# Kernel optimization log

Hardware: AMD Instinct MI355X
Metric: run time of the kernel (lower is better)

## Reference

```python
import jax, jax.numpy as jnp
import numpy as np

DEPTH, DIM, DFF, DT, VOCAB = 3, 512, 2048, 64, 32000
B, L = 2, 512


def setup_inputs() -> dict:
    key = jax.random.key(0)
    ks = jax.random.split(key, 16)
    z = lambda *s: jnp.zeros(s, jnp.float32)
    o = lambda *s: jnp.ones(s, jnp.float32)
    n = lambda k, s, std: jax.random.normal(k, s, jnp.float32) * std
    return {
        "x": jax.random.normal(ks[0], (B, L, VOCAB), jnp.float32),
        "tok_in_w": n(ks[1], (DIM, VOCAB), VOCAB ** -0.5),
        "tok_in_b": z(DIM),
        "ln1_g": o(DEPTH, DIM), "ln1_b": z(DEPTH, DIM),
        "fc_w": n(ks[2], (DEPTH, DT, DIM), DIM ** -0.5), "fc_b": z(DEPTH, DT),
        "tin_w": n(ks[3], (DEPTH, DT, DIM), DIM ** -0.5), "tin_b": z(DEPTH, DT),
        "a_w": n(ks[4], (DEPTH, 2 * DT, DT), DT ** -0.5),
        "h0": jax.random.normal(ks[5], (DEPTH, DT, 2), jnp.float32),
        "tout_w": n(ks[6], (DEPTH, DIM, DT), DT ** -0.5), "tout_b": z(DEPTH, DIM),
        "ln2_g": o(DEPTH, DIM), "ln2_b": z(DEPTH, DIM),
        "ffn_w1": n(ks[7], (DEPTH, DFF, DIM), DIM ** -0.5), "ffn_b1": z(DEPTH, DFF),
        "ffn_w2": n(ks[8], (DEPTH, DIM, DFF), DFF ** -0.5), "ffn_b2": z(DEPTH, DIM),
        "lnf_g": o(DIM), "lnf_b": z(DIM),
        "tok_out_w": n(ks[9], (VOCAB, DIM), DIM ** -0.5), "tok_out_b": z(VOCAB),
    }


def _ln(x, g, b, eps=1e-5):
    m = x.mean(-1, keepdims=True)
    v = jnp.mean((x - m) ** 2, -1, keepdims=True)
    return (x - m) * jax.lax.rsqrt(v + eps) * g + b


def _sioconv(x, a_w, h0):
    # x: (B, L, D). Complex decaying linear recurrence, materialized as the
    # same O(L^2) kernel the torch code builds (cumsum of complex logs replaces
    # the FFT-conv-with-ones, which computes exactly a prefix sum along k).
    Bx, Lx, D = x.shape
    za = (x @ a_w.T).reshape(Bx, Lx, D, 2)
    m2 = za[..., 0] ** 2 + za[..., 1] ** 2
    scale = jax.lax.rsqrt(m2) * jnp.exp(-m2)            # |a| = exp(-|a0|^2)
    a = (za[..., 0] + 1j * za[..., 1]) * scale.astype(jnp.complex64)
    a_ln = jnp.log(a)                                   # (B, L, D)
    S = jnp.cumsum(a_ln, axis=1)
    Sp = jnp.concatenate([jnp.zeros_like(S[:, :1]), S[:, :-1]], axis=1)
    # diff[b,i,k,d] = sum_{j=i..k} a_ln[b,j,d]
    diff = S[:, None, :, :] - Sp[:, :, None, :]          # (B, i, k, D)
    idx = jnp.arange(Lx)
    mask = (idx[None, :] >= idx[:, None] - 1)[None, :, :, None]  # triu(diag=-1)
    c = jnp.where(mask, jnp.exp(jnp.where(mask, diff, 0.0)), 0.0)
    h0c = h0[:, 0] + 1j * h0[:, 1]                       # (D,) complex init state
    xc = x.astype(jnp.complex64)
    xs = jnp.concatenate([jnp.broadcast_to(h0c, (Bx, 1, D)), xc[:, :-1]], axis=1)
    h = jnp.einsum('bikd,bkd->bid', c, xs)               # (B, L, D) complex
    h = h.at[:, -1].add(xc[:, -1])
    return h.real.astype(x.dtype)


def _block(x, p):
    (g1, b1, fcw, fcb, tiw, tib, aw, h0, tow, tob, g2, b2, w1, fb1, w2, fb2) = p
    r = x
    xn = _ln(x, g1, b1)
    y = jax.nn.silu(xn @ fcw.T + fcb)                    # gate (B, L, DT)
    t = _sioconv(xn @ tiw.T + tib, aw, h0)
    x = (t * y) @ tow.T + tob + r
    r = x
    xn = _ln(x, g2, b2)
    return jax.nn.silu(xn @ w1.T + fb1) @ w2.T + fb2 + r


def reference(x, tok_in_w, tok_in_b, ln1_g, ln1_b, fc_w, fc_b, tin_w, tin_b, a_w, h0, tout_w, tout_b, ln2_g, ln2_b, ffn_w1, ffn_b1, ffn_w2, ffn_b2, lnf_g, lnf_b, tok_out_w, tok_out_b):
    h = x @ tok_in_w.T + tok_in_b
    for i in range(DEPTH):
        p = (ln1_g[i], ln1_b[i], fc_w[i], fc_b[i], tin_w[i], tin_b[i], a_w[i], h0[i],
             tout_w[i], tout_b[i], ln2_g[i], ln2_b[i], ffn_w1[i], ffn_b1[i], ffn_w2[i], ffn_b2[i])
        h = _block(h, p)
    h = _ln(h, lnf_g, lnf_b)
    return h @ tok_out_w.T + tok_out_b
```

## Files before the change

### kernel.cpp

```cpp
#include <hip/hip_runtime.h>
#include <hip/hip_bf16.h>


#define LDIM 512
#define SEQL 512
#define DT_ 64
#define NC 16
#define CL 32
#define BK 32

typedef short s16x4 __attribute__((ext_vector_type(4)));
typedef short s16x8 __attribute__((ext_vector_type(8)));
typedef float f32x4 __attribute__((ext_vector_type(4)));

__device__ __forceinline__ unsigned short f2bf(float f) {
  unsigned u = __builtin_bit_cast(unsigned, f);
  return (unsigned short)((u + 0x7fffu + ((u >> 16) & 1u)) >> 16);
}

__device__ __forceinline__ void split2(float f, short& hi, short& lo) {
  unsigned u = __builtin_bit_cast(unsigned, f);
  hi = (short)(u >> 16);
  float hf = __builtin_bit_cast(float, u & 0xFFFF0000u);
  float lf = f - hf;
  lo = (short)(__builtin_bit_cast(unsigned, lf) >> 16);
}

template <int BM, int BN, int ACT, bool RES, bool ATOM, bool BIAS, bool SPL,
          int AACT = 0, bool WBF = false, bool SWZ = false, bool DUAL = false>
__global__ __launch_bounds__(256) void gemm_bt(
    const float* __restrict__ A, const float* __restrict__ W,
    const float* __restrict__ bias, const float* __restrict__ R,
    float* __restrict__ C, int M, int N, int K, int kc,
    const float* __restrict__ W2, const float* __restrict__ bias2,
    float* __restrict__ C2) {
  constexpr int WM = BM / 2, WN = BN / 2, TM = WM / 16, TN = WN / 16;
  constexpr int LDA = BK + 8;
  constexpr int PLANES = SPL ? 2 : 1;
  __shared__ __align__(16) short As[BM * LDA * PLANES];
  __shared__ __align__(16) short Bs[BN * LDA * PLANES];

  const int tid = threadIdx.x;
  const int wid = tid >> 6, lane = tid & 63;
  const int q = lane >> 4, l16 = lane & 15;
  const int wm = (wid >> 1) * WM, wn = (wid & 1) * WN;

  int bx, by, bz;
  if constexpr (SWZ) {
    int b = blockIdx.x;
    by = b & 7; bx = (b >> 3) & 3; bz = b >> 5;
  } else {
    bx = blockIdx.x; by = blockIdx.y; bz = blockIdx.z;
  }
  if constexpr (DUAL) {
    if (bx) { W = W2; bias = bias2; C = C2; }
    bx = 0;
  }
  const int m0 = by * BM, n0 = bx * BN;
  const int kbeg = bz * kc;
  const int kend = min(K, kbeg + kc);

  f32x4 acc[TM][TN] = {};

  constexpr int AF = BM * BK / 1024;
  constexpr int BF = BN * BK / 1024;

  for (int k0 = kbeg; k0 < kend; k0 += BK) {
#pragma unroll
    for (int t = 0; t < AF; t++) {
      int fi = tid + t * 256;
      int row = fi >> 3, col = (fi & 7) << 2;
      float4 v = *(const float4*)(A + (size_t)(m0 + row) * K + k0 + col);
      float* vp = (float*)&v;
      s16x4 hv, lv;
#pragma unroll
      for (int c = 0; c < 4; c++) {
        if (AACT == 1) vp[c] = vp[c] / (1.f + __expf(-vp[c]));
        if (SPL) {
          short h_, l_;
          split2(vp[c], h_, l_);
          hv[c] = h_; lv[c] = l_;
        } else {
          hv[c] = (short)f2bf(vp[c]);
        }
      }
      *(s16x4*)(&As[row * LDA + col]) = hv;
      if (SPL) *(s16x4*)(&As[BM * LDA + row * LDA + col]) = lv;
    }
    if constexpr (WBF) {
      const short* Wb = (const short*)W;
      constexpr int BF2 = BN / 64;
#pragma unroll
      for (int t = 0; t < BF2; t++) {
        int fi = tid + t * 256;
        int row = fi >> 2, col8 = (fi & 3) << 3;
        s16x8 v = *(const s16x8*)(Wb + (size_t)(n0 + row) * K + k0 + col8);
        *(s16x8*)(&Bs[row * LDA + col8]) = v;
      }
    } else {
#pragma unroll
      for (int t = 0; t < BF; t++) {
        int fi = tid + t * 256;
        int row = fi >> 3, col = (fi & 7) << 2;
        float4 v = *(const float4*)(W + (size_t)(n0 + row) * K + k0 + col);
        const float* vp = (const float*)&v;
        s16x4 hv, lv;
#pragma unroll
        for (int c = 0; c < 4; c++) {
          if (SPL) {
            short h_, l_;
            split2(vp[c], h_, l_);
            hv[c] = h_; lv[c] = l_;
          } else {
            hv[c] = (short)f2bf(vp[c]);
          }
        }
        *(s16x4*)(&Bs[row * LDA + col]) = hv;
        if (SPL) *(s16x4*)(&Bs[BN * LDA + row * LDA + col]) = lv;
      }
    }
    __syncthreads();
    s16x8 ah[TM], bh[TN], al[TM], bl[TN];
#pragma unroll
    for (int i = 0; i < TM; i++) {
      ah[i] = *(const s16x8*)(&As[(wm + i * 16 + l16) * LDA + q * 8]);
      if (SPL) al[i] = *(const s16x8*)(&As[BM * LDA + (wm + i * 16 + l16) * LDA + q * 8]);
    }
#pragma unroll
    for (int j = 0; j < TN; j++) {
      bh[j] = *(const s16x8*)(&Bs[(wn + j * 16 + l16) * LDA + q * 8]);
      if (SPL) bl[j] = *(const s16x8*)(&Bs[BN * LDA + (wn + j * 16 + l16) * LDA + q * 8]);
    }
#pragma unroll
    for (int i = 0; i < TM; i++)
#pragma unroll
      for (int j = 0; j < TN; j++) {
        acc[i][j] = __builtin_amdgcn_mfma_f32_16x16x32_bf16(ah[i], bh[j], acc[i][j], 0, 0, 0);
        if (SPL) {
          acc[i][j] = __builtin_amdgcn_mfma_f32_16x16x32_bf16(ah[i], bl[j], acc[i][j], 0, 0, 0);
          acc[i][j] = __builtin_amdgcn_mfma_f32_16x16x32_bf16(al[i], bh[j], acc[i][j], 0, 0, 0);
        }
      }
    __syncthreads();
  }

#pragma unroll
  for (int i = 0; i < TM; i++)
#pragma unroll
    for (int j = 0; j < TN; j++)
#pragma unroll
      for (int r = 0; r < 4; r++) {
        int m = m0 + wm + i * 16 + q * 4 + r;
        int n = n0 + wn + j * 16 + l16;
        float v = acc[i][j][r];
        if (BIAS && kbeg == 0) v += bias[n];
        if (ACT == 1) v = v / (1.f + __expf(-v));
        if (RES) v += R[(size_t)m * N + n];
        if (ATOM) atomicAdd(&C[(size_t)m * N + n], v);
        else C[(size_t)m * N + n] = v;
      }
}

__global__ __launch_bounds__(256) void fill0(float* __restrict__ p) {
  size_t i = (size_t)(blockIdx.x * 256 + threadIdx.x) * 4;
  *(float4*)(p + i) = make_float4(0.f, 0.f, 0.f, 0.f);
}

__global__ __launch_bounds__(256) void cvt_rne(const float* __restrict__ src,
                                               short* __restrict__ dst) {
  size_t i = (size_t)(blockIdx.x * 256 + threadIdx.x) * 4;
  float4 v = *(const float4*)(src + i);
  const float* vp = (const float*)&v;
  s16x4 o;
#pragma unroll
  for (int c = 0; c < 4; c++) o[c] = (short)f2bf(vp[c]);
  *(s16x4*)(dst + i) = o;
}

__global__ __launch_bounds__(256) void ln512(const float* __restrict__ x,
                                             const float* __restrict__ g,
                                             const float* __restrict__ b,
                                             float* __restrict__ o) {
  int wid = threadIdx.x >> 6, lane = threadIdx.x & 63;
  int row = blockIdx.x * 4 + wid;
  const float* xr = x + (size_t)row * 512 + lane * 8;
  float4 v0 = *(const float4*)xr;
  float4 v1 = *(const float4*)(xr + 4);
  float s = v0.x + v0.y + v0.z + v0.w + v1.x + v1.y + v1.z + v1.w;
  float ss = v0.x * v0.x + v0.y * v0.y + v0.z * v0.z + v0.w * v0.w +
             v1.x * v1.x + v1.y * v1.y + v1.z * v1.z + v1.w * v1.w;
#pragma unroll
  for (int m = 32; m; m >>= 1) { s += __shfl_xor(s, m); ss += __shfl_xor(ss, m); }
  float mean = s * (1.f / 512.f);
  float var = ss * (1.f / 512.f) - mean * mean;
  float rstd = rsqrtf(var + 1e-5f);
  const float* gp = g + lane * 8;
  const float* bp = b + lane * 8;
  float4 g0 = *(const float4*)gp, g1 = *(const float4*)(gp + 4);
  float4 b0 = *(const float4*)bp, b1 = *(const float4*)(bp + 4);
  float* op = o + (size_t)row * 512 + lane * 8;
  float4 r0, r1;
  r0.x = (v0.x - mean) * rstd * g0.x + b0.x;
  r0.y = (v0.y - mean) * rstd * g0.y + b0.y;
  r0.z = (v0.z - mean) * rstd * g0.z + b0.z;
  r0.w = (v0.w - mean) * rstd * g0.w + b0.w;
  r1.x = (v1.x - mean) * rstd * g1.x + b1.x;
  r1.y = (v1.y - mean) * rstd * g1.y + b1.y;
  r1.z = (v1.z - mean) * rstd * g1.z + b1.z;
  r1.w = (v1.w - mean) * rstd * g1.w + b1.w;
  *(float4*)op = r0;
  *(float4*)(op + 4) = r1;
}

__device__ __forceinline__ float2 a_of(const float* __restrict__ za, int b, int i, int d) {
  float zr = za[(size_t)(b * SEQL + i) * 128 + 2 * d];
  float zi = za[(size_t)(b * SEQL + i) * 128 + 2 * d + 1];
  float m2 = zr * zr + zi * zi;
  float sc = rsqrtf(m2) * __expf(-m2);
  return make_float2(zr * sc, zi * sc);
}

__device__ __forceinline__ float2 xsm1_of(const float* __restrict__ u,
                                          const float* __restrict__ h0,
                                          int b, int i, int d) {
  if (i == 0) return make_float2(0.f, 0.f);
  if (i == 1) return make_float2(h0[d * 2], h0[d * 2 + 1]);
  return make_float2(u[(size_t)(b * SEQL + i - 2) * DT_ + d], 0.f);
}

__global__ __launch_bounds__(1024) void scan_all(const float* __restrict__ za,
                                                 const float* __restrict__ u,
                                                 const float* __restrict__ h0,
                                                 const float* __restrict__ y,
                                                 float* __restrict__ p) {
  __shared__ float2 sA[NC * 64], sB[NC * 64], sT[NC * 64];
  const int b = blockIdx.x;
  const int t = threadIdx.x;
  const int d = t & 63, c = t >> 6;

  float2 Aa = make_float2(1.f, 0.f), Bv = make_float2(0.f, 0.f);
  for (int i = c * CL + CL - 1; i >= c * CL; i--) {
    float2 a = a_of(za, b, i, d);
    float2 xs = xsm1_of(u, h0, b, i, d);
    float2 nb, nA;
    nb.x = xs.x + a.x * Bv.x - a.y * Bv.y;
    nb.y = xs.y + a.x * Bv.y + a.y * Bv.x;
    nA.x = a.x * Aa.x - a.y * Aa.y;
    nA.y = a.x * Aa.y + a.y * Aa.x;
    Bv = nb; Aa = nA;
  }
  sA[c * 64 + d] = Aa;
  sB[c * 64 + d] = Bv;
  __syncthreads();

  if (c == 0) {
    float2 tt = make_float2(u[(size_t)(b * SEQL + SEQL - 2) * DT_ + d], 0.f);
    for (int cc = NC - 1; cc >= 0; cc--) {
      sT[cc * 64 + d] = tt;
      float2 A = sA[cc * 64 + d], Bc = sB[cc * 64 + d];
      float2 nt;
      nt.x = A.x * tt.x - A.y * tt.y + Bc.x;
      nt.y = A.x * tt.y + A.y * tt.x + Bc.y;
      tt = nt;
    }
  }
  __syncthreads();

  float2 tt = sT[c * 64 + d];
  for (int i = c * CL + CL - 1; i >= c * CL; i--) {
    float2 a = a_of(za, b, i, d);
    float2 xs = xsm1_of(u, h0, b, i, d);
    float2 nt;
    nt.x = xs.x + a.x * tt.x - a.y * tt.y;
    nt.y = xs.y + a.x * tt.y + a.y * tt.x;
    tt = nt;
    float hr = tt.x;
    if (i == SEQL - 1) hr += u[(size_t)(b * SEQL + SEQL - 1) * DT_ + d];
    size_t o = (size_t)(b * SEQL + i) * DT_ + d;
    float yv = y[o];
    yv = yv / (1.f + __expf(-yv));
    p[o] = hr * yv;
  }
}

extern "C" void kernel_launch(void* const* d_in, const int* in_sizes, int n_in,
                              void* d_out, int out_size, void* d_ws, size_t ws_size,
                              hipStream_t stream) {
  const float* x        = (const float*)d_in[0];
  const float* tok_in_w = (const float*)d_in[1];
  const float* tok_in_b = (const float*)d_in[2];
  const float* ln1_g    = (const float*)d_in[3];
  const float* ln1_b    = (const float*)d_in[4];
  const float* fc_w     = (const float*)d_in[5];
  const float* fc_b     = (const float*)d_in[6];
  const float* tin_w    = (const float*)d_in[7];
  const float* tin_b    = (const float*)d_in[8];
  const float* a_w      = (const float*)d_in[9];
  const float* h0       = (const float*)d_in[10];
  const float* tout_w   = (const float*)d_in[11];
  const float* tout_b   = (const float*)d_in[12];
  const float* ln2_g    = (const float*)d_in[13];
  const float* ln2_b    = (const float*)d_in[14];
  const float* ffn_w1   = (const float*)d_in[15];
  const float* ffn_b1   = (const float*)d_in[16];
  const float* ffn_w2   = (const float*)d_in[17];
  const float* ffn_b2   = (const float*)d_in[18];
  const float* lnf_g    = (const float*)d_in[19];
  const float* lnf_b    = (const float*)d_in[20];
  const float* tok_out_w = (const float*)d_in[21];
  const float* tok_out_b = (const float*)d_in[22];
  float* out = (float*)d_out;

  float* ws = (float*)d_ws;
  float* h  = ws;
  float* xn = h + 524288;
  float* y  = xn + 524288;
  float* u  = y + 65536;
  float* za = u + 65536;
  float* p  = za + 131072;
  float* f1 = p + 65536;
  short* wb = (short*)(f1 + 2097152);
  const bool use_wbf = ws_size >= (size_t)(3473408 + 8192000) * 4;

  dim3 blk(256);

  fill0<<<512, blk, 0, stream>>>(h);
  gemm_bt<128, 128, 0, false, true, true, true, 0, false, true>
      <<<dim3(1024), blk, 0, stream>>>(
      x, tok_in_w, tok_in_b, nullptr, h, 1024, 512, 32000, 1024,
      nullptr, nullptr, nullptr);

  for (int l = 0; l < 3; l++) {
    ln512<<<256, blk, 0, stream>>>(h, ln1_g + l * 512, ln1_b + l * 512, xn);
    fill0<<<128, blk, 0, stream>>>(y);
    gemm_bt<64, 64, 0, false, true, true, true, 0, false, false, true>
        <<<dim3(2, 16, 4), blk, 0, stream>>>(
        xn, fc_w + l * 32768, fc_b + l * 64, nullptr, y, 1024, 64, 512, 128,
        tin_w + l * 32768, tin_b + l * 64, u);
    gemm_bt<64, 64, 0, false, false, false, true><<<dim3(2, 16, 1), blk, 0, stream>>>(
        u, a_w + l * 8192, nullptr, nullptr, za, 1024, 128, 64, 64,
        nullptr, nullptr, nullptr);
    scan_all<<<2, 1024, 0, stream>>>(za, u, h0 + l * 128, y, p);
    gemm_bt<64, 128, 0, true, false, true, true><<<dim3(4, 16, 1), blk, 0, stream>>>(
        p, tout_w + l * 32768, tout_b + l * 512, h, h, 1024, 512, 64, 64,
        nullptr, nullptr, nullptr);
    ln512<<<256, blk, 0, stream>>>(h, ln2_g + l * 512, ln2_b + l * 512, xn);
    fill0<<<2048, blk, 0, stream>>>(f1);
    gemm_bt<128, 128, 0, false, true, true, true><<<dim3(16, 8, 2), blk, 0, stream>>>(
        xn, ffn_w1 + l * 1048576, ffn_b1 + l * 2048, nullptr, f1, 1024, 2048, 512, 256,
        nullptr, nullptr, nullptr);
    gemm_bt<128, 128, 0, false, true, true, true, 1><<<dim3(4, 8, 8), blk, 0, stream>>>(
        f1, ffn_w2 + l * 1048576, ffn_b2 + l * 512, nullptr, h, 1024, 512, 2048, 256,
        nullptr, nullptr, nullptr);
  }

  ln512<<<256, blk, 0, stream>>>(h, lnf_g, lnf_b, xn);
  if (use_wbf) {
    cvt_rne<<<16000, blk, 0, stream>>>(tok_out_w, wb);
    gemm_bt<128, 128, 0, false, false, true, false, 0, true>
        <<<dim3(250, 8, 1), blk, 0, stream>>>(
        xn, (const float*)wb, tok_out_b, nullptr, out, 1024, 32000, 512, 512,
        nullptr, nullptr, nullptr);
  } else {
    gemm_bt<128, 128, 0, false, false, true, false><<<dim3(250, 8, 1), blk, 0, stream>>>(
        xn, tok_out_w, tok_out_b, nullptr, out, 1024, 32000, 512, 512,
        nullptr, nullptr, nullptr);
  }
}
```

Baseline: 1.114 ms.

## Prefetch next GEMM k-tile into registers and split chunked scan into three kernels

```diff
diff --git a/kernel.cpp b/kernel.cpp
--- a/kernel.cpp
+++ b/kernel.cpp
@@ -27,7 +27,7 @@
 }
 
 template <int BM, int BN, int ACT, bool RES, bool ATOM, bool BIAS, bool SPL,
-          int AACT = 0, bool WBF = false, bool SWZ = false, bool DUAL = false>
+          int AACT = 0, bool WBF = false, bool DUAL = false>
 __global__ __launch_bounds__(256) void gemm_bt(
     const float* __restrict__ A, const float* __restrict__ W,
     const float* __restrict__ bias, const float* __restrict__ R,
@@ -45,13 +45,7 @@
   const int q = lane >> 4, l16 = lane & 15;
   const int wm = (wid >> 1) * WM, wn = (wid & 1) * WN;
 
-  int bx, by, bz;
-  if constexpr (SWZ) {
-    int b = blockIdx.x;
-    by = b & 7; bx = (b >> 3) & 3; bz = b >> 5;
-  } else {
-    bx = blockIdx.x; by = blockIdx.y; bz = blockIdx.z;
-  }
+  int bx = blockIdx.x, by = blockIdx.y, bz = blockIdx.z;
   if constexpr (DUAL) {
     if (bx) { W = W2; bias = bias2; C = C2; }
     bx = 0;
@@ -64,13 +58,44 @@
 
   constexpr int AF = BM * BK / 1024;
   constexpr int BF = BN * BK / 1024;
-
-  for (int k0 = kbeg; k0 < kend; k0 += BK) {
+  constexpr int WF = WBF ? (BN / 64) : 1;
+
+  float4 pa[AF];
+  float4 pb[WBF ? 1 : BF];
+  s16x8 pw[WF];
+
+  auto load_a = [&](int k0) {
 #pragma unroll
     for (int t = 0; t < AF; t++) {
       int fi = tid + t * 256;
       int row = fi >> 3, col = (fi & 7) << 2;
-      float4 v = *(const float4*)(A + (size_t)(m0 + row) * K + k0 + col);
+      pa[t] = *(const float4*)(A + (size_t)(m0 + row) * K + k0 + col);
+    }
+  };
+  auto load_b = [&](int k0) {
+    if constexpr (WBF) {
+      const short* Wb = (const short*)W;
+#pragma unroll
+      for (int t = 0; t < WF; t++) {
+        int fi = tid + t * 256;
+        int row = fi >> 2, col8 = (fi & 3) << 3;
+        pw[t] = *(const s16x8*)(Wb + (size_t)(n0 + row) * K + k0 + col8);
+      }
+    } else {
+#pragma unroll
+      for (int t = 0; t < BF; t++) {
+        int fi = tid + t * 256;
+        int row = fi >> 3, col = (fi & 7) << 2;
+        pb[t] = *(const float4*)(W + (size_t)(n0 + row) * K + k0 + col);
+      }
+    }
+  };
+  auto store_tiles = [&]() {
+#pragma unroll
+    for (int t = 0; t < AF; t++) {
+      int fi = tid + t * 256;
+      int row = fi >> 3, col = (fi & 7) << 2;
+      float4 v = pa[t];
       float* vp = (float*)&v;
       s16x4 hv, lv;
 #pragma unroll
@@ -88,21 +113,18 @@
       if (SPL) *(s16x4*)(&As[BM * LDA + row * LDA + col]) = lv;
     }
     if constexpr (WBF) {
-      const short* Wb = (const short*)W;
-      constexpr int BF2 = BN / 64;
-#pragma unroll
-      for (int t = 0; t < BF2; t++) {
+#pragma unroll
+      for (int t = 0; t < WF; t++) {
         int fi = tid + t * 256;
         int row = fi >> 2, col8 = (fi & 3) << 3;
-        s16x8 v = *(const s16x8*)(Wb + (size_t)(n0 + row) * K + k0 + col8);
-        *(s16x8*)(&Bs[row * LDA + col8]) = v;
+        *(s16x8*)(&Bs[row * LDA + col8]) = pw[t];
       }
     } else {
 #pragma unroll
       for (int t = 0; t < BF; t++) {
         int fi = tid + t * 256;
         int row = fi >> 3, col = (fi & 7) << 2;
-        float4 v = *(const float4*)(W + (size_t)(n0 + row) * K + k0 + col);
+        float4 v = pb[t];
         const float* vp = (const float*)&v;
         s16x4 hv, lv;
 #pragma unroll
@@ -119,7 +141,17 @@
         if (SPL) *(s16x4*)(&Bs[BN * LDA + row * LDA + col]) = lv;
       }
     }
+  };
+
+  load_a(kbeg);
+  load_b(kbeg);
+  for (int k0 = kbeg; k0 < kend; k0 += BK) {
+    store_tiles();
     __syncthreads();
+    if (k0 + BK < kend) {
+      load_a(k0 + BK);
+      load_b(k0 + BK);
+    }
     s16x8 ah[TM], bh[TN], al[TM], bl[TN];
 #pragma unroll
     for (int i = 0; i < TM; i++) {
@@ -228,16 +260,13 @@
   return make_float2(u[(size_t)(b * SEQL + i - 2) * DT_ + d], 0.f);
 }
 
-__global__ __launch_bounds__(1024) void scan_all(const float* __restrict__ za,
-                                                 const float* __restrict__ u,
-                                                 const float* __restrict__ h0,
-                                                 const float* __restrict__ y,
-                                                 float* __restrict__ p) {
-  __shared__ float2 sA[NC * 64], sB[NC * 64], sT[NC * 64];
-  const int b = blockIdx.x;
-  const int t = threadIdx.x;
-  const int d = t & 63, c = t >> 6;
-
+__global__ __launch_bounds__(256) void scan_p1(const float* __restrict__ za,
+                                               const float* __restrict__ u,
+                                               const float* __restrict__ h0,
+                                               float2* __restrict__ cA,
+                                               float2* __restrict__ cB) {
+  int tid = blockIdx.x * 256 + threadIdx.x;
+  int d = tid & 63, c = (tid >> 6) & (NC - 1), b = tid >> 10;
   float2 Aa = make_float2(1.f, 0.f), Bv = make_float2(0.f, 0.f);
   for (int i = c * CL + CL - 1; i >= c * CL; i--) {
     float2 a = a_of(za, b, i, d);
@@ -249,32 +278,45 @@
     nA.y = a.x * Aa.y + a.y * Aa.x;
     Bv = nb; Aa = nA;
   }
-  sA[c * 64 + d] = Aa;
-  sB[c * 64 + d] = Bv;
-  __syncthreads();
-
-  if (c == 0) {
-    float2 tt = make_float2(u[(size_t)(b * SEQL + SEQL - 2) * DT_ + d], 0.f);
-    for (int cc = NC - 1; cc >= 0; cc--) {
-      sT[cc * 64 + d] = tt;
-      float2 A = sA[cc * 64 + d], Bc = sB[cc * 64 + d];
-      float2 nt;
-      nt.x = A.x * tt.x - A.y * tt.y + Bc.x;
-      nt.y = A.x * tt.y + A.y * tt.x + Bc.y;
-      tt = nt;
-    }
-  }
-  __syncthreads();
-
-  float2 tt = sT[c * 64 + d];
+  cA[tid] = Aa;
+  cB[tid] = Bv;
+}
+
+__global__ __launch_bounds__(128) void scan_p2(const float* __restrict__ u,
+                                               const float2* __restrict__ cA,
+                                               const float2* __restrict__ cB,
+                                               float2* __restrict__ tE) {
+  int tid = threadIdx.x;
+  int d = tid & 63, b = tid >> 6;
+  float2 t = make_float2(u[(size_t)(b * SEQL + SEQL - 2) * DT_ + d], 0.f);
+  for (int c = NC - 1; c >= 0; c--) {
+    int idx = (b << 10) + (c << 6) + d;
+    tE[idx] = t;
+    float2 A = cA[idx], Bv = cB[idx];
+    float2 nt;
+    nt.x = A.x * t.x - A.y * t.y + Bv.x;
+    nt.y = A.x * t.y + A.y * t.x + Bv.y;
+    t = nt;
+  }
+}
+
+__global__ __launch_bounds__(256) void scan_p3(const float* __restrict__ za,
+                                               const float* __restrict__ u,
+                                               const float* __restrict__ h0,
+                                               const float* __restrict__ y,
+                                               const float2* __restrict__ tE,
+                                               float* __restrict__ p) {
+  int tid = blockIdx.x * 256 + threadIdx.x;
+  int d = tid & 63, c = (tid >> 6) & (NC - 1), b = tid >> 10;
+  float2 t = tE[tid];
   for (int i = c * CL + CL - 1; i >= c * CL; i--) {
     float2 a = a_of(za, b, i, d);
     float2 xs = xsm1_of(u, h0, b, i, d);
     float2 nt;
-    nt.x = xs.x + a.x * tt.x - a.y * tt.y;
-    nt.y = xs.y + a.x * tt.y + a.y * tt.x;
-    tt = nt;
-    float hr = tt.x;
+    nt.x = xs.x + a.x * t.x - a.y * t.y;
+    nt.y = xs.y + a.x * t.y + a.y * t.x;
+    t = nt;
+    float hr = t.x;
     if (i == SEQL - 1) hr += u[(size_t)(b * SEQL + SEQL - 1) * DT_ + d];
     size_t o = (size_t)(b * SEQL + i) * DT_ + d;
     float yv = y[o];
@@ -319,28 +361,32 @@
   float* za = u + 65536;
   float* p  = za + 131072;
   float* f1 = p + 65536;
-  short* wb = (short*)(f1 + 2097152);
-  const bool use_wbf = ws_size >= (size_t)(3473408 + 8192000) * 4;
+  float2* cA = (float2*)(f1 + 2097152);
+  float2* cB = cA + 2048;
+  float2* tE = cB + 2048;
+  short* wb = (short*)(tE + 2048);
+  const bool use_wbf = ws_size >= (size_t)(3485696 + 8192000) * 4;
 
   dim3 blk(256);
 
   fill0<<<512, blk, 0, stream>>>(h);
-  gemm_bt<128, 128, 0, false, true, true, true, 0, false, true>
-      <<<dim3(1024), blk, 0, stream>>>(
+  gemm_bt<128, 128, 0, false, true, true, true><<<dim3(4, 8, 32), blk, 0, stream>>>(
       x, tok_in_w, tok_in_b, nullptr, h, 1024, 512, 32000, 1024,
       nullptr, nullptr, nullptr);
 
   for (int l = 0; l < 3; l++) {
     ln512<<<256, blk, 0, stream>>>(h, ln1_g + l * 512, ln1_b + l * 512, xn);
     fill0<<<128, blk, 0, stream>>>(y);
-    gemm_bt<64, 64, 0, false, true, true, true, 0, false, false, true>
+    gemm_bt<64, 64, 0, false, true, true, true, 0, false, true>
         <<<dim3(2, 16, 4), blk, 0, stream>>>(
         xn, fc_w + l * 32768, fc_b + l * 64, nullptr, y, 1024, 64, 512, 128,
         tin_w + l * 32768, tin_b + l * 64, u);
     gemm_bt<64, 64, 0, false, false, false, true><<<dim3(2, 16, 1), blk, 0, stream>>>(
         u, a_w + l * 8192, nullptr, nullptr, za, 1024, 128, 64, 64,
         nullptr, nullptr, nullptr);
-    scan_all<<<2, 1024, 0, stream>>>(za, u, h0 + l * 128, y, p);
+    scan_p1<<<8, blk, 0, stream>>>(za, u, h0 + l * 128, cA, cB);
+    scan_p2<<<1, 128, 0, stream>>>(u, cA, cB, tE);
+    scan_p3<<<8, blk, 0, stream>>>(za, u, h0 + l * 128, y, tE, p);
     gemm_bt<64, 128, 0, true, false, true, true><<<dim3(4, 16, 1), blk, 0, stream>>>(
         p, tout_w + l * 32768, tout_b + l * 512, h, h, 1024, 512, 64, 64,
         nullptr, nullptr, nullptr);
```

Measured after the change: 1.065 ms. 4.3% less time.
